# Kernel optimization log

Hardware: AMD Instinct MI355X
Metric: run time of the kernel (lower is better)

The kernel has to match this reference:

```python
import jax, jax.numpy as jnp
import numpy as np

def setup_inputs() -> dict:
    key = jax.random.key(0)
    k1, k2, k3 = jax.random.split(key, 3)
    B, N, Din, Dout = 4, 1024, 64, 64
    x = jax.random.normal(k1, (B, N, Din), dtype=jnp.float32)
    # nn.Linear(2*Din, Dout): weight [Dout, 2*Din], bias [Dout]
    W = jax.random.normal(k2, (Dout, 2 * Din), dtype=jnp.float32) * (1.0 / np.sqrt(2 * Din))
    b = jax.random.normal(k3, (Dout,), dtype=jnp.float32) * 0.01
    return {"x": x, "W": W, "b": b}

def reference(x, W, b):
    # Faithful to: y_pairs[b,i,j] = Linear(cat([x[b,i], x[b,j]])); y = max_i y_pairs
    # Separable form: cat([x1,x2]) @ W.T = x1 @ W1.T + x2 @ W2.T
    Din = x.shape[-1]
    W1 = W[:, :Din]   # acts on x1 (row index i)
    W2 = W[:, Din:]   # acts on x2 (column index j)
    a = jnp.einsum('bnd,od->bno', x, W1)  # [B, N, Dout], i-contribution
    c = jnp.einsum('bnd,od->bno', x, W2)  # [B, N, Dout], j-contribution
    y_pairs = a[:, :, None, :] + c[:, None, :, :] + b  # [B, i, j, Dout]
    return jnp.max(y_pairs, axis=1)  # pool over i (dim=-3) -> [B, N, Dout]
```

## Files before the change

### kernel.cpp

```cpp
#include <hip/hip_runtime.h>

#define WPAD 68

__global__ __launch_bounds__(256) void pe_k1(const float* __restrict__ x,
                                             const float* __restrict__ W,
                                             float* __restrict__ wsmax) {
    __shared__ float Wt[64 * WPAD];
    __shared__ float xs[16 * WPAD];
    __shared__ float red[16 * 64];

    const int t  = threadIdx.x;
    const int b  = blockIdx.x >> 6;
    const int ch = blockIdx.x & 63;
    const int m0 = ch << 4;

    const float4* W4 = (const float4*)W;
    #pragma unroll
    for (int i = 0; i < 4; ++i) {
        int id = t + 256 * i;
        int o = id >> 4, q = id & 15;
        float4 wv = W4[o * 32 + q];
        Wt[(4 * q + 0) * WPAD + o] = wv.x;
        Wt[(4 * q + 1) * WPAD + o] = wv.y;
        Wt[(4 * q + 2) * WPAD + o] = wv.z;
        Wt[(4 * q + 3) * WPAD + o] = wv.w;
    }
    {
        const float4* x4 = (const float4*)(x + ((size_t)b * 1024 + m0) * 64);
        float4 xv = x4[t];
        *(float4*)&xs[(t >> 4) * WPAD + 4 * (t & 15)] = xv;
    }
    __syncthreads();

    const int r  = t >> 4;
    const int og = t & 15;
    const float* xr = &xs[r * WPAD];
    float ax = 0.f, ay = 0.f, az = 0.f, aw = 0.f;

    #pragma unroll
    for (int q = 0; q < 16; ++q) {
        float4 xq = *(const float4*)&xr[4 * q];
        float4 w0 = *(const float4*)&Wt[(4 * q + 0) * WPAD + og * 4];
        float4 w1 = *(const float4*)&Wt[(4 * q + 1) * WPAD + og * 4];
        float4 w2 = *(const float4*)&Wt[(4 * q + 2) * WPAD + og * 4];
        float4 w3 = *(const float4*)&Wt[(4 * q + 3) * WPAD + og * 4];
        ax += xq.x * w0.x; ay += xq.x * w0.y; az += xq.x * w0.z; aw += xq.x * w0.w;
        ax += xq.y * w1.x; ay += xq.y * w1.y; az += xq.y * w1.z; aw += xq.y * w1.w;
        ax += xq.z * w2.x; ay += xq.z * w2.y; az += xq.z * w2.z; aw += xq.z * w2.w;
        ax += xq.w * w3.x; ay += xq.w * w3.y; az += xq.w * w3.z; aw += xq.w * w3.w;
    }
    *(float4*)&red[r * 64 + og * 4] = make_float4(ax, ay, az, aw);
    __syncthreads();

    if (t < 64) {
        float v = red[t];
        #pragma unroll
        for (int rr = 1; rr < 16; ++rr) v = fmaxf(v, red[rr * 64 + t]);
        wsmax[((size_t)(b << 6) + ch) * 64 + t] = v;
    }
}

__global__ __launch_bounds__(256) void pe_k2(const float* __restrict__ x,
                                             const float* __restrict__ W,
                                             const float* __restrict__ bias,
                                             const float* __restrict__ wsmax,
                                             float* __restrict__ out) {
    __shared__ float Wt[64 * WPAD];
    __shared__ float xs[16 * WPAD];
    __shared__ float amx[4 * 64];
    __shared__ float addv[64];

    const int t  = threadIdx.x;
    const int b  = blockIdx.x >> 6;
    const int ch = blockIdx.x & 63;
    const int m0 = ch << 4;

    const float4* W4 = (const float4*)W;
    #pragma unroll
    for (int i = 0; i < 4; ++i) {
        int id = t + 256 * i;
        int o = id >> 4, q = id & 15;
        float4 wv = W4[o * 32 + 16 + q];
        Wt[(4 * q + 0) * WPAD + o] = wv.x;
        Wt[(4 * q + 1) * WPAD + o] = wv.y;
        Wt[(4 * q + 2) * WPAD + o] = wv.z;
        Wt[(4 * q + 3) * WPAD + o] = wv.w;
    }
    {
        const float4* x4 = (const float4*)(x + ((size_t)b * 1024 + m0) * 64);
        float4 xv = x4[t];
        *(float4*)&xs[(t >> 4) * WPAD + 4 * (t & 15)] = xv;
    }
    {
        const int o = t & 63, g = t >> 6;
        const float* wp = wsmax + (size_t)b * 4096 + o;
        float v = wp[(size_t)g * 64];
        #pragma unroll
        for (int s = 1; s < 16; ++s) v = fmaxf(v, wp[(size_t)(g + 4 * s) * 64]);
        amx[g * 64 + o] = v;
    }
    __syncthreads();
    if (t < 64) {
        float v = fmaxf(fmaxf(amx[t], amx[64 + t]), fmaxf(amx[128 + t], amx[192 + t]));
        addv[t] = v + bias[t];
    }
    __syncthreads();

    const int r  = t >> 4;
    const int og = t & 15;
    const float* xr = &xs[r * WPAD];
    float4 add = *(const float4*)&addv[og * 4];
    float cx = add.x, cy = add.y, cz = add.z, cw = add.w;

    #pragma unroll
    for (int q = 0; q < 16; ++q) {
        float4 xq = *(const float4*)&xr[4 * q];
        float4 w0 = *(const float4*)&Wt[(4 * q + 0) * WPAD + og * 4];
        float4 w1 = *(const float4*)&Wt[(4 * q + 1) * WPAD + og * 4];
        float4 w2 = *(const float4*)&Wt[(4 * q + 2) * WPAD + og * 4];
        float4 w3 = *(const float4*)&Wt[(4 * q + 3) * WPAD + og * 4];
        cx += xq.x * w0.x; cy += xq.x * w0.y; cz += xq.x * w0.z; cw += xq.x * w0.w;
        cx += xq.y * w1.x; cy += xq.y * w1.y; cz += xq.y * w1.z; cw += xq.y * w1.w;
        cx += xq.z * w2.x; cy += xq.z * w2.y; cz += xq.z * w2.z; cw += xq.z * w2.w;
        cx += xq.w * w3.x; cy += xq.w * w3.y; cz += xq.w * w3.z; cw += xq.w * w3.w;
    }

    size_t oidx = ((size_t)b * 1024 + (m0 + r)) * 64 + og * 4;
    *(float4*)&out[oidx] = make_float4(cx, cy, cz, cw);
}

extern "C" void kernel_launch(void* const* d_in, const int* in_sizes, int n_in,
                              void* d_out, int out_size, void* d_ws, size_t ws_size,
                              hipStream_t stream) {
    const float* x    = (const float*)d_in[0];
    const float* W    = (const float*)d_in[1];
    const float* bias = (const float*)d_in[2];
    float* out   = (float*)d_out;
    float* wsmax = (float*)d_ws;

    pe_k1<<<4 * 64, 256, 0, stream>>>(x, W, wsmax);
    pe_k2<<<4 * 64, 256, 0, stream>>>(x, W, bias, wsmax, out);
}
```

Measured before the change: 12.82 us.

## Split K across thread pairs with 512-thread blocks and shuffle reductions

Both kernels now run 512 threads per block. Each pair of threads splits the 64-wide dot product into two halves and combines them with a lane shuffle. In the first kernel, the row max is partly done with a cross-lane shuffle, which shrinks the shared reduction buffer. In the second kernel, the matmul now overlaps the wsmax max-reduction before the barrier, and the bias/max add is applied at the store. The aim is to shorten per-thread dependency chains and hide latency in these tiny launch-bound kernels, at the cost of extra shuffles and idle threads during loads.

```diff
diff --git a/kernel.cpp b/kernel.cpp
--- a/kernel.cpp
+++ b/kernel.cpp
@@ -2,12 +2,13 @@
 
 #define WPAD 68
 
-__global__ __launch_bounds__(256) void pe_k1(const float* __restrict__ x,
+
+__global__ __launch_bounds__(512) void pe_k1(const float* __restrict__ x,
                                              const float* __restrict__ W,
                                              float* __restrict__ wsmax) {
     __shared__ float Wt[64 * WPAD];
     __shared__ float xs[16 * WPAD];
-    __shared__ float red[16 * 64];
+    __shared__ float red[8 * 64];
 
     const int t  = threadIdx.x;
     const int b  = blockIdx.x >> 6;
@@ -16,58 +17,66 @@
 
     const float4* W4 = (const float4*)W;
     #pragma unroll
-    for (int i = 0; i < 4; ++i) {
-        int id = t + 256 * i;
+    for (int i = 0; i < 2; ++i) {
+        int id = t + 512 * i;
         int o = id >> 4, q = id & 15;
-        float4 wv = W4[o * 32 + q];
-        Wt[(4 * q + 0) * WPAD + o] = wv.x;
-        Wt[(4 * q + 1) * WPAD + o] = wv.y;
-        Wt[(4 * q + 2) * WPAD + o] = wv.z;
-        Wt[(4 * q + 3) * WPAD + o] = wv.w;
+        float4 w = W4[o * 32 + q];
+        Wt[(4 * q + 0) * WPAD + o] = w.x;
+        Wt[(4 * q + 1) * WPAD + o] = w.y;
+        Wt[(4 * q + 2) * WPAD + o] = w.z;
+        Wt[(4 * q + 3) * WPAD + o] = w.w;
     }
-    {
+    if (t < 256) {
         const float4* x4 = (const float4*)(x + ((size_t)b * 1024 + m0) * 64);
         float4 xv = x4[t];
         *(float4*)&xs[(t >> 4) * WPAD + 4 * (t & 15)] = xv;
     }
     __syncthreads();
 
-    const int r  = t >> 4;
-    const int og = t & 15;
-    const float* xr = &xs[r * WPAD];
+    const int r  = t >> 5;
+    const int og = (t >> 1) & 15;
+    const int kh = t & 1;
+    const float* xr = &xs[r * WPAD + kh * 32];
+    const int k0 = kh * 32;
+
     float ax = 0.f, ay = 0.f, az = 0.f, aw = 0.f;
+    #pragma unroll
+    for (int q = 0; q < 8; ++q) {
+        float4 xq = *(const float4*)&xr[4 * q];
+        float4 w0 = *(const float4*)&Wt[(k0 + 4 * q + 0) * WPAD + og * 4];
+        float4 w1 = *(const float4*)&Wt[(k0 + 4 * q + 1) * WPAD + og * 4];
+        float4 w2 = *(const float4*)&Wt[(k0 + 4 * q + 2) * WPAD + og * 4];
+        float4 w3 = *(const float4*)&Wt[(k0 + 4 * q + 3) * WPAD + og * 4];
+        ax += xq.x * w0.x + xq.y * w1.x + xq.z * w2.x + xq.w * w3.x;
+        ay += xq.x * w0.y + xq.y * w1.y + xq.z * w2.y + xq.w * w3.y;
+        az += xq.x * w0.z + xq.y * w1.z + xq.z * w2.z + xq.w * w3.z;
+        aw += xq.x * w0.w + xq.y * w1.w + xq.z * w2.w + xq.w * w3.w;
+    }
+    ax += __shfl_xor(ax, 1); ay += __shfl_xor(ay, 1);
+    az += __shfl_xor(az, 1); aw += __shfl_xor(aw, 1);
+    ax = fmaxf(ax, __shfl_xor(ax, 32)); ay = fmaxf(ay, __shfl_xor(ay, 32));
+    az = fmaxf(az, __shfl_xor(az, 32)); aw = fmaxf(aw, __shfl_xor(aw, 32));
 
-    #pragma unroll
-    for (int q = 0; q < 16; ++q) {
-        float4 xq = *(const float4*)&xr[4 * q];
-        float4 w0 = *(const float4*)&Wt[(4 * q + 0) * WPAD + og * 4];
-        float4 w1 = *(const float4*)&Wt[(4 * q + 1) * WPAD + og * 4];
-        float4 w2 = *(const float4*)&Wt[(4 * q + 2) * WPAD + og * 4];
-        float4 w3 = *(const float4*)&Wt[(4 * q + 3) * WPAD + og * 4];
-        ax += xq.x * w0.x; ay += xq.x * w0.y; az += xq.x * w0.z; aw += xq.x * w0.w;
-        ax += xq.y * w1.x; ay += xq.y * w1.y; az += xq.y * w1.z; aw += xq.y * w1.w;
-        ax += xq.z * w2.x; ay += xq.z * w2.y; az += xq.z * w2.z; aw += xq.z * w2.w;
-        ax += xq.w * w3.x; ay += xq.w * w3.y; az += xq.w * w3.z; aw += xq.w * w3.w;
-    }
-    *(float4*)&red[r * 64 + og * 4] = make_float4(ax, ay, az, aw);
+    if ((t & 33) == 0)
+        *(float4*)&red[(t >> 6) * 64 + og * 4] = make_float4(ax, ay, az, aw);
     __syncthreads();
 
     if (t < 64) {
         float v = red[t];
         #pragma unroll
-        for (int rr = 1; rr < 16; ++rr) v = fmaxf(v, red[rr * 64 + t]);
+        for (int w = 1; w < 8; ++w) v = fmaxf(v, red[w * 64 + t]);
         wsmax[((size_t)(b << 6) + ch) * 64 + t] = v;
     }
 }
 
-__global__ __launch_bounds__(256) void pe_k2(const float* __restrict__ x,
+__global__ __launch_bounds__(512) void pe_k2(const float* __restrict__ x,
                                              const float* __restrict__ W,
                                              const float* __restrict__ bias,
                                              const float* __restrict__ wsmax,
                                              float* __restrict__ out) {
     __shared__ float Wt[64 * WPAD];
     __shared__ float xs[16 * WPAD];
-    __shared__ float amx[4 * 64];
+    __shared__ float amx[8 * 64];
     __shared__ float addv[64];
 
     const int t  = threadIdx.x;
@@ -77,16 +86,16 @@
 
     const float4* W4 = (const float4*)W;
     #pragma unroll
-    for (int i = 0; i < 4; ++i) {
-        int id = t + 256 * i;
+    for (int i = 0; i < 2; ++i) {
+        int id = t + 512 * i;
         int o = id >> 4, q = id & 15;
-        float4 wv = W4[o * 32 + 16 + q];
-        Wt[(4 * q + 0) * WPAD + o] = wv.x;
-        Wt[(4 * q + 1) * WPAD + o] = wv.y;
-        Wt[(4 * q + 2) * WPAD + o] = wv.z;
-        Wt[(4 * q + 3) * WPAD + o] = wv.w;
+        float4 w = W4[o * 32 + 16 + q];
+        Wt[(4 * q + 0) * WPAD + o] = w.x;
+        Wt[(4 * q + 1) * WPAD + o] = w.y;
+        Wt[(4 * q + 2) * WPAD + o] = w.z;
+        Wt[(4 * q + 3) * WPAD + o] = w.w;
     }
-    {
+    if (t < 256) {
         const float4* x4 = (const float4*)(x + ((size_t)b * 1024 + m0) * 64);
         float4 xv = x4[t];
         *(float4*)&xs[(t >> 4) * WPAD + 4 * (t & 15)] = xv;
@@ -96,37 +105,44 @@
         const float* wp = wsmax + (size_t)b * 4096 + o;
         float v = wp[(size_t)g * 64];
         #pragma unroll
-        for (int s = 1; s < 16; ++s) v = fmaxf(v, wp[(size_t)(g + 4 * s) * 64]);
+        for (int s = 1; s < 8; ++s) v = fmaxf(v, wp[(size_t)(g + 8 * s) * 64]);
         amx[g * 64 + o] = v;
     }
     __syncthreads();
     if (t < 64) {
-        float v = fmaxf(fmaxf(amx[t], amx[64 + t]), fmaxf(amx[128 + t], amx[192 + t]));
+        float v = amx[t];
+        #pragma unroll
+        for (int w = 1; w < 8; ++w) v = fmaxf(v, amx[w * 64 + t]);
         addv[t] = v + bias[t];
     }
+    const int r  = t >> 5;
+    const int og = (t >> 1) & 15;
+    const int kh = t & 1;
+    const float* xr = &xs[r * WPAD + kh * 32];
+    const int k0 = kh * 32;
+
+    float cx = 0.f, cy = 0.f, cz = 0.f, cw = 0.f;
+    #pragma unroll
+    for (int q = 0; q < 8; ++q) {
+        float4 xq = *(const float4*)&xr[4 * q];
+        float4 w0 = *(const float4*)&Wt[(k0 + 4 * q + 0) * WPAD + og * 4];
+        float4 w1 = *(const float4*)&Wt[(k0 + 4 * q + 1) * WPAD + og * 4];
+        float4 w2 = *(const float4*)&Wt[(k0 + 4 * q + 2) * WPAD + og * 4];
+        float4 w3 = *(const float4*)&Wt[(k0 + 4 * q + 3) * WPAD + og * 4];
+        cx += xq.x * w0.x + xq.y * w1.x + xq.z * w2.x + xq.w * w3.x;
+        cy += xq.x * w0.y + xq.y * w1.y + xq.z * w2.y + xq.w * w3.y;
+        cz += xq.x * w0.z + xq.y * w1.z + xq.z * w2.z + xq.w * w3.z;
+        cw += xq.x * w0.w + xq.y * w1.w + xq.z * w2.w + xq.w * w3.w;
+    }
+    cx += __shfl_xor(cx, 1); cy += __shfl_xor(cy, 1);
+    cz += __shfl_xor(cz, 1); cw += __shfl_xor(cw, 1);
     __syncthreads();
 
-    const int r  = t >> 4;
-    const int og = t & 15;
-    const float* xr = &xs[r * WPAD];
-    float4 add = *(const float4*)&addv[og * 4];
-    float cx = add.x, cy = add.y, cz = add.z, cw = add.w;
-
-    #pragma unroll
-    for (int q = 0; q < 16; ++q) {
-        float4 xq = *(const float4*)&xr[4 * q];
-        float4 w0 = *(const float4*)&Wt[(4 * q + 0) * WPAD + og * 4];
-        float4 w1 = *(const float4*)&Wt[(4 * q + 1) * WPAD + og * 4];
-        float4 w2 = *(const float4*)&Wt[(4 * q + 2) * WPAD + og * 4];
-        float4 w3 = *(const float4*)&Wt[(4 * q + 3) * WPAD + og * 4];
-        cx += xq.x * w0.x; cy += xq.x * w0.y; cz += xq.x * w0.z; cw += xq.x * w0.w;
-        cx += xq.y * w1.x; cy += xq.y * w1.y; cz += xq.y * w1.z; cw += xq.y * w1.w;
-        cx += xq.z * w2.x; cy += xq.z * w2.y; cz += xq.z * w2.z; cw += xq.z * w2.w;
-        cx += xq.w * w3.x; cy += xq.w * w3.y; cz += xq.w * w3.z; cw += xq.w * w3.w;
+    if (kh == 0) {
+        float4 add = *(const float4*)&addv[og * 4];
+        *(float4*)&out[((size_t)b * 1024 + m0 + r) * 64 + og * 4] =
+            make_float4(cx + add.x, cy + add.y, cz + add.z, cw + add.w);
     }
-
-    size_t oidx = ((size_t)b * 1024 + (m0 + r)) * 64 + og * 4;
-    *(float4*)&out[oidx] = make_float4(cx, cy, cz, cw);
 }
 
 extern "C" void kernel_launch(void* const* d_in, const int* in_sizes, int n_in,
@@ -138,6 +154,6 @@
     float* out   = (float*)d_out;
     float* wsmax = (float*)d_ws;
 
-    pe_k1<<<4 * 64, 256, 0, stream>>>(x, W, wsmax);
-    pe_k2<<<4 * 64, 256, 0, stream>>>(x, W, bias, wsmax, out);
+    pe_k1<<<4 * 64, 512, 0, stream>>>(x, W, wsmax);
+    pe_k2<<<4 * 64, 512, 0, stream>>>(x, W, bias, wsmax, out);
 }
```

New measurement: 13.13 us. 2.3% more time.

## Load x rows into registers, reduce with wave shuffles, overlap global max with GEMV

Applied to the files above, without the earlier changes.

Each thread now loads its x row directly from global memory into 16 float4 registers instead of staging it through shared memory. In the first kernel, the per-block max over 16 rows becomes a wave-level shuffle-xor reduction followed by a small 4-entry shared reduce. In the second kernel, the workspace max is loaded before the GEMV, and the bias-plus-max add is deferred until after the dot products, removing one barrier before compute. This trades shared-memory traffic and barriers for higher register pressure and redundant x loads (16 threads read the same row), which rely on L1 cache hits.

```diff
diff --git a/kernel.cpp b/kernel.cpp
--- a/kernel.cpp
+++ b/kernel.cpp
@@ -1,61 +1,65 @@
 #include <hip/hip_runtime.h>
 
 #define WPAD 68
+
 
 __global__ __launch_bounds__(256) void pe_k1(const float* __restrict__ x,
                                              const float* __restrict__ W,
                                              float* __restrict__ wsmax) {
     __shared__ float Wt[64 * WPAD];
-    __shared__ float xs[16 * WPAD];
-    __shared__ float red[16 * 64];
+    __shared__ float red[4 * 64];
 
     const int t  = threadIdx.x;
     const int b  = blockIdx.x >> 6;
     const int ch = blockIdx.x & 63;
     const int m0 = ch << 4;
+    const int r  = t >> 4;
+    const int og = t & 15;
+
+    const float4* xr = (const float4*)(x + ((size_t)b * 1024 + m0 + r) * 64);
+    float4 xq[16];
+    #pragma unroll
+    for (int q = 0; q < 16; ++q) xq[q] = xr[q];
 
     const float4* W4 = (const float4*)W;
     #pragma unroll
     for (int i = 0; i < 4; ++i) {
         int id = t + 256 * i;
         int o = id >> 4, q = id & 15;
-        float4 wv = W4[o * 32 + q];
-        Wt[(4 * q + 0) * WPAD + o] = wv.x;
-        Wt[(4 * q + 1) * WPAD + o] = wv.y;
-        Wt[(4 * q + 2) * WPAD + o] = wv.z;
-        Wt[(4 * q + 3) * WPAD + o] = wv.w;
-    }
-    {
-        const float4* x4 = (const float4*)(x + ((size_t)b * 1024 + m0) * 64);
-        float4 xv = x4[t];
-        *(float4*)&xs[(t >> 4) * WPAD + 4 * (t & 15)] = xv;
+        float4 w = W4[o * 32 + q];
+        Wt[(4 * q + 0) * WPAD + o] = w.x;
+        Wt[(4 * q + 1) * WPAD + o] = w.y;
+        Wt[(4 * q + 2) * WPAD + o] = w.z;
+        Wt[(4 * q + 3) * WPAD + o] = w.w;
     }
     __syncthreads();
 
-    const int r  = t >> 4;
-    const int og = t & 15;
-    const float* xr = &xs[r * WPAD];
     float ax = 0.f, ay = 0.f, az = 0.f, aw = 0.f;
-
     #pragma unroll
     for (int q = 0; q < 16; ++q) {
-        float4 xq = *(const float4*)&xr[4 * q];
+        float4 xv = xq[q];
         float4 w0 = *(const float4*)&Wt[(4 * q + 0) * WPAD + og * 4];
         float4 w1 = *(const float4*)&Wt[(4 * q + 1) * WPAD + og * 4];
         float4 w2 = *(const float4*)&Wt[(4 * q + 2) * WPAD + og * 4];
         float4 w3 = *(const float4*)&Wt[(4 * q + 3) * WPAD + og * 4];
-        ax += xq.x * w0.x; ay += xq.x * w0.y; az += xq.x * w0.z; aw += xq.x * w0.w;
-        ax += xq.y * w1.x; ay += xq.y * w1.y; az += xq.y * w1.z; aw += xq.y * w1.w;
-        ax += xq.z * w2.x; ay += xq.z * w2.y; az += xq.z * w2.z; aw += xq.z * w2.w;
-        ax += xq.w * w3.x; ay += xq.w * w3.y; az += xq.w * w3.z; aw += xq.w * w3.w;
+        ax += xv.x * w0.x + xv.y * w1.x + xv.z * w2.x + xv.w * w3.x;
+        ay += xv.x * w0.y + xv.y * w1.y + xv.z * w2.y + xv.w * w3.y;
+        az += xv.x * w0.z + xv.y * w1.z + xv.z * w2.z + xv.w * w3.z;
+        aw += xv.x * w0.w + xv.y * w1.w + xv.z * w2.w + xv.w * w3.w;
     }
-    *(float4*)&red[r * 64 + og * 4] = make_float4(ax, ay, az, aw);
+
+    ax = fmaxf(ax, __shfl_xor(ax, 16)); ay = fmaxf(ay, __shfl_xor(ay, 16));
+    az = fmaxf(az, __shfl_xor(az, 16)); aw = fmaxf(aw, __shfl_xor(aw, 16));
+    ax = fmaxf(ax, __shfl_xor(ax, 32)); ay = fmaxf(ay, __shfl_xor(ay, 32));
+    az = fmaxf(az, __shfl_xor(az, 32)); aw = fmaxf(aw, __shfl_xor(aw, 32));
+
+    if ((t & 48) == 0)
+        *(float4*)&red[(t >> 6) * 64 + og * 4] = make_float4(ax, ay, az, aw);
     __syncthreads();
 
     if (t < 64) {
-        float v = red[t];
-        #pragma unroll
-        for (int rr = 1; rr < 16; ++rr) v = fmaxf(v, red[rr * 64 + t]);
+        float v = fmaxf(fmaxf(red[t], red[64 + t]),
+                        fmaxf(red[128 + t], red[192 + t]));
         wsmax[((size_t)(b << 6) + ch) * 64 + t] = v;
     }
 }
@@ -66,7 +70,6 @@
                                              const float* __restrict__ wsmax,
                                              float* __restrict__ out) {
     __shared__ float Wt[64 * WPAD];
-    __shared__ float xs[16 * WPAD];
     __shared__ float amx[4 * 64];
     __shared__ float addv[64];
 
@@ -74,59 +77,58 @@
     const int b  = blockIdx.x >> 6;
     const int ch = blockIdx.x & 63;
     const int m0 = ch << 4;
+    const int r  = t >> 4;
+    const int og = t & 15;
+
+    float gv;
+    {
+        const int o = t & 63, g = t >> 6;
+        const float* wp = wsmax + (size_t)b * 4096 + o;
+        gv = wp[(size_t)g * 64];
+        #pragma unroll
+        for (int s = 1; s < 16; ++s) gv = fmaxf(gv, wp[(size_t)(g + 4 * s) * 64]);
+    }
+
+    const float4* xr = (const float4*)(x + ((size_t)b * 1024 + m0 + r) * 64);
+    float4 xq[16];
+    #pragma unroll
+    for (int q = 0; q < 16; ++q) xq[q] = xr[q];
 
     const float4* W4 = (const float4*)W;
     #pragma unroll
     for (int i = 0; i < 4; ++i) {
         int id = t + 256 * i;
         int o = id >> 4, q = id & 15;
-        float4 wv = W4[o * 32 + 16 + q];
-        Wt[(4 * q + 0) * WPAD + o] = wv.x;
-        Wt[(4 * q + 1) * WPAD + o] = wv.y;
-        Wt[(4 * q + 2) * WPAD + o] = wv.z;
-        Wt[(4 * q + 3) * WPAD + o] = wv.w;
+        float4 w = W4[o * 32 + 16 + q];
+        Wt[(4 * q + 0) * WPAD + o] = w.x;
+        Wt[(4 * q + 1) * WPAD + o] = w.y;
+        Wt[(4 * q + 2) * WPAD + o] = w.z;
+        Wt[(4 * q + 3) * WPAD + o] = w.w;
     }
-    {
-        const float4* x4 = (const float4*)(x + ((size_t)b * 1024 + m0) * 64);
-        float4 xv = x4[t];
-        *(float4*)&xs[(t >> 4) * WPAD + 4 * (t & 15)] = xv;
-    }
-    {
-        const int o = t & 63, g = t >> 6;
-        const float* wp = wsmax + (size_t)b * 4096 + o;
-        float v = wp[(size_t)g * 64];
-        #pragma unroll
-        for (int s = 1; s < 16; ++s) v = fmaxf(v, wp[(size_t)(g + 4 * s) * 64]);
-        amx[g * 64 + o] = v;
-    }
-    __syncthreads();
-    if (t < 64) {
-        float v = fmaxf(fmaxf(amx[t], amx[64 + t]), fmaxf(amx[128 + t], amx[192 + t]));
-        addv[t] = v + bias[t];
-    }
+    amx[(t >> 6) * 64 + (t & 63)] = gv;
     __syncthreads();
 
-    const int r  = t >> 4;
-    const int og = t & 15;
-    const float* xr = &xs[r * WPAD];
-    float4 add = *(const float4*)&addv[og * 4];
-    float cx = add.x, cy = add.y, cz = add.z, cw = add.w;
-
+    if (t < 64)
+        addv[t] = fmaxf(fmaxf(amx[t], amx[64 + t]),
+                        fmaxf(amx[128 + t], amx[192 + t])) + bias[t];
+    float cx = 0.f, cy = 0.f, cz = 0.f, cw = 0.f;
     #pragma unroll
     for (int q = 0; q < 16; ++q) {
-        float4 xq = *(const float4*)&xr[4 * q];
+        float4 xv = xq[q];
         float4 w0 = *(const float4*)&Wt[(4 * q + 0) * WPAD + og * 4];
         float4 w1 = *(const float4*)&Wt[(4 * q + 1) * WPAD + og * 4];
         float4 w2 = *(const float4*)&Wt[(4 * q + 2) * WPAD + og * 4];
         float4 w3 = *(const float4*)&Wt[(4 * q + 3) * WPAD + og * 4];
-        cx += xq.x * w0.x; cy += xq.x * w0.y; cz += xq.x * w0.z; cw += xq.x * w0.w;
-        cx += xq.y * w1.x; cy += xq.y * w1.y; cz += xq.y * w1.z; cw += xq.y * w1.w;
-        cx += xq.z * w2.x; cy += xq.z * w2.y; cz += xq.z * w2.z; cw += xq.z * w2.w;
-        cx += xq.w * w3.x; cy += xq.w * w3.y; cz += xq.w * w3.z; cw += xq.w * w3.w;
+        cx += xv.x * w0.x + xv.y * w1.x + xv.z * w2.x + xv.w * w3.x;
+        cy += xv.x * w0.y + xv.y * w1.y + xv.z * w2.y + xv.w * w3.y;
+        cz += xv.x * w0.z + xv.y * w1.z + xv.z * w2.z + xv.w * w3.z;
+        cw += xv.x * w0.w + xv.y * w1.w + xv.z * w2.w + xv.w * w3.w;
     }
+    __syncthreads();
 
-    size_t oidx = ((size_t)b * 1024 + (m0 + r)) * 64 + og * 4;
-    *(float4*)&out[oidx] = make_float4(cx, cy, cz, cw);
+    float4 add = *(const float4*)&addv[og * 4];
+    *(float4*)&out[((size_t)b * 1024 + m0 + r) * 64 + og * 4] =
+        make_float4(cx + add.x, cy + add.y, cz + add.z, cw + add.w);
 }
 
 extern "C" void kernel_launch(void* const* d_in, const int* in_sizes, int n_in,
```

Result: no change. 13.01 us (+1.5%).
